# Optimization experiments

Hardware: AMD Instinct MI355X
Metric: run time of the kernel (lower is better)

Reference implementation:

```python
import jax, jax.numpy as jnp
import numpy as np

N = 50000
E = 625000
D_IN = 128
D_OUT = 128


def setup_inputs() -> dict:
    key = jax.random.key(0)
    k1, k2, k3, k4 = jax.random.split(key, 4)
    x = jax.random.normal(k1, (N, D_IN), dtype=jnp.float32)
    edge_index = jax.random.randint(k2, (2, E), 0, N, dtype=jnp.int64)
    edge_weight = jax.random.uniform(k3, (E,), dtype=jnp.float32)
    # xavier_uniform with gain=0.05: limit = gain * sqrt(6/(fan_in+fan_out))
    limit = 0.05 * np.sqrt(6.0 / (D_IN + D_OUT))
    weight = jax.random.uniform(k4, (D_OUT, D_IN), dtype=jnp.float32,
                                minval=-limit, maxval=limit)
    bias = jnp.zeros((D_OUT,), dtype=jnp.float32)
    return {"x": x, "edge_index": edge_index, "edge_weight": edge_weight,
            "weight": weight, "bias": bias}


def reference(x, edge_index, edge_weight, weight, bias):
    src = edge_index[0]
    dst = edge_index[1]
    # gather source features and weight per edge: [E, D_IN]
    msg = x[src] * edge_weight[:, None]
    # scatter-add into destination nodes: [N, D_IN]
    agg = jax.ops.segment_sum(msg, dst, num_segments=x.shape[0])
    # linear + bias + relu
    h = agg @ weight.T + bias
    return jax.nn.relu(h)
```

## Files before the change

### kernel.cpp

```cpp
#include <hip/hip_runtime.h>
#include <hip/hip_fp16.h>

#define NN 50000
#define NE 625000
#define D  128
#define CAP 64
#define NBIN 196
#define BCAP 4096
#define BIN_BLOCKS 200
#define BIN_CHUNK 3125
#define GBM 128
#define XC_BLKS 3125
#define K2_X  NBIN
#define K2_W  (NBIN + XC_BLKS)
#define K2_GRID (K2_W + 8)

typedef __attribute__((ext_vector_type(8))) short bf16x8;
typedef __attribute__((ext_vector_type(4))) float f32x4;

__device__ inline unsigned f2bf_rne(float f) {
    unsigned u = __float_as_uint(f);
    u += 0x7FFFu + ((u >> 16) & 1u);
    return u >> 16;
}

__device__ inline unsigned pack_hi(float a, float b, float& ra, float& rb) {
    unsigned ba = __float_as_uint(a) & 0xffff0000u;
    unsigned bb = __float_as_uint(b) & 0xffff0000u;
    ra = a - __uint_as_float(ba);
    rb = b - __uint_as_float(bb);
    return (ba >> 16) | bb;
}
__device__ inline unsigned pack_lo(float ra, float rb) {
    return (__float_as_uint(ra) >> 16) | (__float_as_uint(rb) & 0xffff0000u);
}

__global__ __launch_bounds__(256) void bin_coarse(const int* __restrict__ src,
                                                  const int* __restrict__ dst,
                                                  const float* __restrict__ ew,
                                                  int* __restrict__ binc,
                                                  uint2* __restrict__ binbuf,
                                                  int* __restrict__ ovf_cnt,
                                                  uint2* __restrict__ ovf) {
    __shared__ int hcnt[4][NBIN];
    __shared__ int hbase4[4][NBIN];
    __shared__ int hcur4[4][NBIN];
    const int tid = threadIdx.x;
    const int wv = tid >> 6;
    const int e0 = blockIdx.x * BIN_CHUNK;
    const int e1 = min(e0 + BIN_CHUNK, NE);

    for (int i = tid; i < NBIN; i += 256) {
        hcnt[0][i] = 0; hcnt[1][i] = 0; hcnt[2][i] = 0; hcnt[3][i] = 0;
    }
    __syncthreads();
    for (int e = e0 + tid; e < e1; e += 256)
        atomicAdd(&hcnt[wv][dst[e] >> 8], 1);
    __syncthreads();
    for (int i = tid; i < NBIN; i += 256) {
        int c0 = hcnt[0][i], c1 = hcnt[1][i], c2 = hcnt[2][i], c3 = hcnt[3][i];
        int tot = c0 + c1 + c2 + c3;
        int base = tot ? atomicAdd(&binc[i], tot) : 0;
        hbase4[0][i] = base;
        hbase4[1][i] = base + c0;
        hbase4[2][i] = base + c0 + c1;
        hbase4[3][i] = base + c0 + c1 + c2;
        hcur4[0][i] = 0; hcur4[1][i] = 0; hcur4[2][i] = 0; hcur4[3][i] = 0;
    }
    __syncthreads();
    for (int e = e0 + tid; e < e1; e += 256) {
        int d = dst[e];
        int bin = d >> 8;
        unsigned entry = ((unsigned)src[e] << 16) |
                         (unsigned)__half_as_ushort(__float2half(ew[e]));
        int slot = hbase4[wv][bin] + atomicAdd(&hcur4[wv][bin], 1);
        if (slot < BCAP) {
            binbuf[(size_t)bin * BCAP + slot] = make_uint2((unsigned)d, entry);
        } else {
            int o = atomicAdd(ovf_cnt, 1);
            ovf[o] = make_uint2((unsigned)d, entry);
        }
    }
}

__global__ __launch_bounds__(256) void k2(const float* __restrict__ x,
                                          const float* __restrict__ W,
                                          const int* __restrict__ binc,
                                          const uint2* __restrict__ binbuf,
                                          int* __restrict__ fillc,
                                          unsigned* __restrict__ buck,
                                          unsigned* __restrict__ xb,
                                          ushort* __restrict__ wsp,
                                          int* __restrict__ ovf_cnt,
                                          uint2* __restrict__ ovf) {
    const int tid = threadIdx.x;
    if (blockIdx.x < K2_X) {
        __shared__ int lcnt[256];
        const int bin = blockIdx.x;
        lcnt[tid] = 0;
        __syncthreads();
        int n = binc[bin];
        if (n > BCAP) n = BCAP;
        const uint2* bp = binbuf + (size_t)bin * BCAP;
        for (int i = tid; i < n; i += 256) {
            uint2 q = bp[i];
            int d = (int)q.x;
            int p = atomicAdd(&lcnt[d & 255], 1);
            if (p < CAP) {
                buck[(size_t)d * CAP + p] = q.y;
            } else {
                int o = atomicAdd(ovf_cnt, 1);
                ovf[o] = q;
            }
        }
        __syncthreads();
        int node = bin * 256 + tid;
        if (node < NN) {
            int c = lcnt[tid];
            if (c > CAP) c = CAP;
            int pc = (c <= 16) ? 16 : ((c + 3) & ~3);
            for (int p = c; p < pc; ++p)
                buck[(size_t)node * CAP + p] = 0;
            fillc[node] = pc;
        }
        return;
    }
    if (blockIdx.x < K2_W) {
        int g = (blockIdx.x - K2_X) * 256 + tid;
        const float4* xp = (const float4*)(x + (size_t)g * 8);
        float4 a = xp[0], b = xp[1];
        uint4 o;
        o.x = f2bf_rne(a.x) | (f2bf_rne(a.y) << 16);
        o.y = f2bf_rne(a.z) | (f2bf_rne(a.w) << 16);
        o.z = f2bf_rne(b.x) | (f2bf_rne(b.y) << 16);
        o.w = f2bf_rne(b.z) | (f2bf_rne(b.w) << 16);
        ((uint4*)xb)[g] = o;
        return;
    }
    int g = (blockIdx.x - K2_W) * 256 + tid;
    if (g >= 128 * 16) return;
    int col = g >> 4;
    int c16 = g & 15;
    const float4* wp = (const float4*)(W + (size_t)col * D + c16 * 8);
    float4 v0 = wp[0], v1 = wp[1];
    float r0, r1, r2, r3, r4, r5, r6, r7;
    uint4 hi, lo;
    hi.x = pack_hi(v0.x, v0.y, r0, r1);
    hi.y = pack_hi(v0.z, v0.w, r2, r3);
    hi.z = pack_hi(v1.x, v1.y, r4, r5);
    hi.w = pack_hi(v1.z, v1.w, r6, r7);
    lo.x = pack_lo(r0, r1); lo.y = pack_lo(r2, r3);
    lo.z = pack_lo(r4, r5); lo.w = pack_lo(r6, r7);
    int sidx = col * 16 + (c16 ^ (col & 15));
    ((uint4*)wsp)[sidx] = hi;
    ((uint4*)(wsp + 16384))[sidx] = lo;
}

__device__ inline float hw(unsigned q) {
    return __half2float(__ushort_as_half((ushort)(q & 0xffffu)));
}

__device__ inline void edge_fma(float4& acc, uint2 u, float wt) {
    acc.x += __uint_as_float(u.x << 16) * wt;
    acc.y += __uint_as_float(u.x & 0xffff0000u) * wt;
    acc.z += __uint_as_float(u.y << 16) * wt;
    acc.w += __uint_as_float(u.y & 0xffff0000u) * wt;
}

__global__ __launch_bounds__(256) void aggregate(const unsigned* __restrict__ xb,
                                                 const int* __restrict__ fillc,
                                                 const unsigned* __restrict__ buck,
                                                 const int* __restrict__ ovf_cnt,
                                                 const uint2* __restrict__ ovf,
                                                 unsigned* __restrict__ aggb) {
    const int node = blockIdx.x * 8 + (threadIdx.x >> 5);
    const int t = threadIdx.x & 31;
    int cnt = fillc[node];
    const uint4* bp4 = (const uint4*)(buck + (size_t)node * CAP);
    const uint2* x2 = (const uint2*)xb;
    float4 acc = {0.f, 0.f, 0.f, 0.f};
    if (cnt <= 16) {
        uint4 q0 = bp4[0], q1 = bp4[1], q2 = bp4[2], q3 = bp4[3];
        uint2 u00 = x2[(size_t)(q0.x >> 16) * 32 + t];
        uint2 u01 = x2[(size_t)(q0.y >> 16) * 32 + t];
        uint2 u02 = x2[(size_t)(q0.z >> 16) * 32 + t];
        uint2 u03 = x2[(size_t)(q0.w >> 16) * 32 + t];
        uint2 u10 = x2[(size_t)(q1.x >> 16) * 32 + t];
        uint2 u11 = x2[(size_t)(q1.y >> 16) * 32 + t];
        uint2 u12 = x2[(size_t)(q1.z >> 16) * 32 + t];
        uint2 u13 = x2[(size_t)(q1.w >> 16) * 32 + t];
        uint2 u20 = x2[(size_t)(q2.x >> 16) * 32 + t];
        uint2 u21 = x2[(size_t)(q2.y >> 16) * 32 + t];
        uint2 u22 = x2[(size_t)(q2.z >> 16) * 32 + t];
        uint2 u23 = x2[(size_t)(q2.w >> 16) * 32 + t];
        uint2 u30 = x2[(size_t)(q3.x >> 16) * 32 + t];
        uint2 u31 = x2[(size_t)(q3.y >> 16) * 32 + t];
        uint2 u32 = x2[(size_t)(q3.z >> 16) * 32 + t];
        uint2 u33 = x2[(size_t)(q3.w >> 16) * 32 + t];
        edge_fma(acc, u00, hw(q0.x)); edge_fma(acc, u01, hw(q0.y));
        edge_fma(acc, u02, hw(q0.z)); edge_fma(acc, u03, hw(q0.w));
        edge_fma(acc, u10, hw(q1.x)); edge_fma(acc, u11, hw(q1.y));
        edge_fma(acc, u12, hw(q1.z)); edge_fma(acc, u13, hw(q1.w));
        edge_fma(acc, u20, hw(q2.x)); edge_fma(acc, u21, hw(q2.y));
        edge_fma(acc, u22, hw(q2.z)); edge_fma(acc, u23, hw(q2.w));
        edge_fma(acc, u30, hw(q3.x)); edge_fma(acc, u31, hw(q3.y));
        edge_fma(acc, u32, hw(q3.z)); edge_fma(acc, u33, hw(q3.w));
    } else {
        int n4 = cnt >> 2;
        for (int i = 0; i < n4; ++i) {
            uint4 q = bp4[i];
            uint2 u0 = x2[(size_t)(q.x >> 16) * 32 + t];
            uint2 u1 = x2[(size_t)(q.y >> 16) * 32 + t];
            uint2 u2 = x2[(size_t)(q.z >> 16) * 32 + t];
            uint2 u3 = x2[(size_t)(q.w >> 16) * 32 + t];
            edge_fma(acc, u0, hw(q.x)); edge_fma(acc, u1, hw(q.y));
            edge_fma(acc, u2, hw(q.z)); edge_fma(acc, u3, hw(q.w));
        }
    }
    int n = *ovf_cnt;
    for (int o = 0; o < n; ++o) {
        uint2 q = ovf[o];
        if ((int)q.x == node) {
            uint2 u = x2[(size_t)(q.y >> 16) * 32 + t];
            edge_fma(acc, u, hw(q.y));
        }
    }
    unsigned o0 = f2bf_rne(acc.x) | (f2bf_rne(acc.y) << 16);
    unsigned o1 = f2bf_rne(acc.z) | (f2bf_rne(acc.w) << 16);
    ((uint2*)aggb)[(size_t)node * 32 + t] = make_uint2(o0, o1);
}

__global__ __launch_bounds__(256) void gemm_mfma(const unsigned* __restrict__ aggb,
                                                 const ushort* __restrict__ wsp,
                                                 const float* __restrict__ bias,
                                                 float* __restrict__ out) {
    __shared__ ushort wl[32768];
    const int tid = threadIdx.x;
    {
        const uint4* s = (const uint4*)wsp;
        uint4* d = (uint4*)wl;
#pragma unroll
        for (int i = 0; i < 16; ++i)
            d[i * 256 + tid] = s[i * 256 + tid];
    }
    __syncthreads();

    const int wid = tid >> 6, lane = tid & 63;
    const int l15 = lane & 15, kg = lane >> 4;
    const int wrbase = blockIdx.x * GBM + wid * 32;

    f32x4 acc[2][8];
    const f32x4 fz = {0.f, 0.f, 0.f, 0.f};
#pragma unroll
    for (int m = 0; m < 2; ++m)
#pragma unroll
        for (int n = 0; n < 8; ++n) acc[m][n] = fz;

    int arow0 = wrbase + l15;
    int arow1 = wrbase + 16 + l15;
    const unsigned* a0p = aggb + (size_t)(arow0 < NN ? arow0 : NN - 1) * 64 + kg * 4;
    const unsigned* a1p = aggb + (size_t)(arow1 < NN ? arow1 : NN - 1) * 64 + kg * 4;

#pragma unroll
    for (int kk = 0; kk < 4; ++kk) {
        uint4 h0 = *(const uint4*)(a0p + kk * 16);
        uint4 h1 = *(const uint4*)(a1p + kk * 16);
        bf16x8 a0 = *(bf16x8*)&h0;
        bf16x8 a1 = *(bf16x8*)&h1;

        int coff = ((kk * 4 + kg) ^ l15) * 8;
#pragma unroll
        for (int nf = 0; nf < 8; ++nf) {
            int bidx = (16 * nf + l15) * 128 + coff;
            bf16x8 bhi = *(const bf16x8*)&wl[bidx];
            bf16x8 blo = *(const bf16x8*)&wl[16384 + bidx];
            acc[0][nf] = __builtin_amdgcn_mfma_f32_16x16x32_bf16(a0, bhi, acc[0][nf], 0, 0, 0);
            acc[1][nf] = __builtin_amdgcn_mfma_f32_16x16x32_bf16(a1, bhi, acc[1][nf], 0, 0, 0);
            acc[0][nf] = __builtin_amdgcn_mfma_f32_16x16x32_bf16(a0, blo, acc[0][nf], 0, 0, 0);
            acc[1][nf] = __builtin_amdgcn_mfma_f32_16x16x32_bf16(a1, blo, acc[1][nf], 0, 0, 0);
        }
    }

    const int rofs = kg * 4;
#pragma unroll
    for (int nf = 0; nf < 8; ++nf) {
        int col = 16 * nf + l15;
        float bv = bias[col];
#pragma unroll
        for (int m = 0; m < 2; ++m) {
#pragma unroll
            for (int r = 0; r < 4; ++r) {
                int row = wrbase + 16 * m + rofs + r;
                if (row < NN) {
                    float h = acc[m][nf][r] + bv;
                    out[(size_t)row * D + col] = h > 0.f ? h : 0.f;
                }
            }
        }
    }
}

extern "C" void kernel_launch(void* const* d_in, const int* in_sizes, int n_in,
                              void* d_out, int out_size, void* d_ws, size_t ws_size,
                              hipStream_t stream) {
    const float* x    = (const float*)d_in[0];
    const int*   eidx = (const int*)d_in[1];
    const float* ew   = (const float*)d_in[2];
    const float* W    = (const float*)d_in[3];
    const float* bias = (const float*)d_in[4];
    float* out = (float*)d_out;

    const int* src = eidx;
    const int* dst = eidx + NE;

    char* base = (char*)d_ws;
    unsigned* aggb   = (unsigned*)base;
    uint2*    binbuf = (uint2*)base;
    unsigned* buck   = (unsigned*)(base + 25600000);
    unsigned* xb     = (unsigned*)(base + 25600000 + 12800000);
    ushort*   wsp    = (ushort*)(base + 51200000);
    int*      fillc   = (int*)(base + 51200000 + 65536);
    int*      binc    = (int*)(base + 51200000 + 65536 + 200000);
    int*      ovf_cnt = (int*)((char*)binc + NBIN * 4);
    uint2*    ovf     = (uint2*)(base + 51200000 + 65536 + 200000 + 1024);

    hipMemsetAsync(binc, 0, NBIN * 4 + 4, stream);
    bin_coarse<<<BIN_BLOCKS, 256, 0, stream>>>(src, dst, ew, binc, binbuf, ovf_cnt, ovf);
    k2<<<K2_GRID, 256, 0, stream>>>(x, W, binc, binbuf, fillc, buck, xb, wsp, ovf_cnt, ovf);
    aggregate<<<6250, 256, 0, stream>>>(xb, fillc, buck, ovf_cnt, ovf, aggb);
    gemm_mfma<<<(NN + GBM - 1) / GBM, 256, 0, stream>>>(aggb, wsp, bias, out);
}
```

Measured before the change: 82.33 us.

## Fuse fine binning into aggregation via LDS buckets and merge coarse binning with conversion

Coarse edge binning now runs in the same launch as the x and W bf16 conversion. The fine per-node bucketing and the gather-aggregate are fused into one kernel per 256-node bin, which keeps the buckets in 64KB of LDS instead of writing and re-reading a global bucket array and fill counts. This removes a kernel launch and the global bucket traffic. The cost is that aggregation now runs on only 196 blocks with large LDS use, which cuts parallelism and occupancy for the gather-heavy phase. Each block also pads its per-node work to rounds of 16 edges.

```diff
diff --git a/kernel.cpp b/kernel.cpp
--- a/kernel.cpp
+++ b/kernel.cpp
@@ -11,9 +11,9 @@
 #define BIN_CHUNK 3125
 #define GBM 128
 #define XC_BLKS 3125
-#define K2_X  NBIN
-#define K2_W  (NBIN + XC_BLKS)
-#define K2_GRID (K2_W + 8)
+#define K1_X  BIN_BLOCKS
+#define K1_W  (BIN_BLOCKS + XC_BLKS)
+#define K1_GRID (K1_W + 8)
 
 typedef __attribute__((ext_vector_type(8))) short bf16x8;
 typedef __attribute__((ext_vector_type(4))) float f32x4;
@@ -35,98 +35,71 @@
     return (__float_as_uint(ra) >> 16) | (__float_as_uint(rb) & 0xffff0000u);
 }
 
-__global__ __launch_bounds__(256) void bin_coarse(const int* __restrict__ src,
-                                                  const int* __restrict__ dst,
-                                                  const float* __restrict__ ew,
-                                                  int* __restrict__ binc,
-                                                  uint2* __restrict__ binbuf,
-                                                  int* __restrict__ ovf_cnt,
-                                                  uint2* __restrict__ ovf) {
-    __shared__ int hcnt[4][NBIN];
-    __shared__ int hbase4[4][NBIN];
-    __shared__ int hcur4[4][NBIN];
-    const int tid = threadIdx.x;
-    const int wv = tid >> 6;
-    const int e0 = blockIdx.x * BIN_CHUNK;
-    const int e1 = min(e0 + BIN_CHUNK, NE);
-
-    for (int i = tid; i < NBIN; i += 256) {
-        hcnt[0][i] = 0; hcnt[1][i] = 0; hcnt[2][i] = 0; hcnt[3][i] = 0;
-    }
-    __syncthreads();
-    for (int e = e0 + tid; e < e1; e += 256)
-        atomicAdd(&hcnt[wv][dst[e] >> 8], 1);
-    __syncthreads();
-    for (int i = tid; i < NBIN; i += 256) {
-        int c0 = hcnt[0][i], c1 = hcnt[1][i], c2 = hcnt[2][i], c3 = hcnt[3][i];
-        int tot = c0 + c1 + c2 + c3;
-        int base = tot ? atomicAdd(&binc[i], tot) : 0;
-        hbase4[0][i] = base;
-        hbase4[1][i] = base + c0;
-        hbase4[2][i] = base + c0 + c1;
-        hbase4[3][i] = base + c0 + c1 + c2;
-        hcur4[0][i] = 0; hcur4[1][i] = 0; hcur4[2][i] = 0; hcur4[3][i] = 0;
-    }
-    __syncthreads();
-    for (int e = e0 + tid; e < e1; e += 256) {
-        int d = dst[e];
-        int bin = d >> 8;
-        unsigned entry = ((unsigned)src[e] << 16) |
-                         (unsigned)__half_as_ushort(__float2half(ew[e]));
-        int slot = hbase4[wv][bin] + atomicAdd(&hcur4[wv][bin], 1);
-        if (slot < BCAP) {
-            binbuf[(size_t)bin * BCAP + slot] = make_uint2((unsigned)d, entry);
-        } else {
-            int o = atomicAdd(ovf_cnt, 1);
-            ovf[o] = make_uint2((unsigned)d, entry);
-        }
-    }
-}
-
-__global__ __launch_bounds__(256) void k2(const float* __restrict__ x,
+__device__ inline float hw(unsigned q) {
+    return __half2float(__ushort_as_half((ushort)(q & 0xffffu)));
+}
+
+__device__ inline void edge_fma(float4& acc, uint2 u, float wt) {
+    acc.x += __uint_as_float(u.x << 16) * wt;
+    acc.y += __uint_as_float(u.x & 0xffff0000u) * wt;
+    acc.z += __uint_as_float(u.y << 16) * wt;
+    acc.w += __uint_as_float(u.y & 0xffff0000u) * wt;
+}
+
+__global__ __launch_bounds__(256) void k1(const float* __restrict__ x,
                                           const float* __restrict__ W,
-                                          const int* __restrict__ binc,
-                                          const uint2* __restrict__ binbuf,
-                                          int* __restrict__ fillc,
-                                          unsigned* __restrict__ buck,
+                                          const int* __restrict__ src,
+                                          const int* __restrict__ dst,
+                                          const float* __restrict__ ew,
                                           unsigned* __restrict__ xb,
                                           ushort* __restrict__ wsp,
+                                          int* __restrict__ binc,
+                                          uint2* __restrict__ binbuf,
                                           int* __restrict__ ovf_cnt,
                                           uint2* __restrict__ ovf) {
     const int tid = threadIdx.x;
-    if (blockIdx.x < K2_X) {
-        __shared__ int lcnt[256];
-        const int bin = blockIdx.x;
-        lcnt[tid] = 0;
+    if (blockIdx.x < K1_X) {
+        __shared__ int hcnt[4][NBIN];
+        __shared__ int hbase4[4][NBIN];
+        __shared__ int hcur4[4][NBIN];
+        const int wv = tid >> 6;
+        const int e0 = blockIdx.x * BIN_CHUNK;
+        const int e1 = min(e0 + BIN_CHUNK, NE);
+        for (int i = tid; i < NBIN; i += 256) {
+            hcnt[0][i] = 0; hcnt[1][i] = 0; hcnt[2][i] = 0; hcnt[3][i] = 0;
+        }
         __syncthreads();
-        int n = binc[bin];
-        if (n > BCAP) n = BCAP;
-        const uint2* bp = binbuf + (size_t)bin * BCAP;
-        for (int i = tid; i < n; i += 256) {
-            uint2 q = bp[i];
-            int d = (int)q.x;
-            int p = atomicAdd(&lcnt[d & 255], 1);
-            if (p < CAP) {
-                buck[(size_t)d * CAP + p] = q.y;
+        for (int e = e0 + tid; e < e1; e += 256)
+            atomicAdd(&hcnt[wv][dst[e] >> 8], 1);
+        __syncthreads();
+        for (int i = tid; i < NBIN; i += 256) {
+            int c0 = hcnt[0][i], c1 = hcnt[1][i], c2 = hcnt[2][i], c3 = hcnt[3][i];
+            int tot = c0 + c1 + c2 + c3;
+            int base = tot ? atomicAdd(&binc[i], tot) : 0;
+            hbase4[0][i] = base;
+            hbase4[1][i] = base + c0;
+            hbase4[2][i] = base + c0 + c1;
+            hbase4[3][i] = base + c0 + c1 + c2;
+            hcur4[0][i] = 0; hcur4[1][i] = 0; hcur4[2][i] = 0; hcur4[3][i] = 0;
+        }
+        __syncthreads();
+        for (int e = e0 + tid; e < e1; e += 256) {
+            int d = dst[e];
+            int bin = d >> 8;
+            unsigned entry = ((unsigned)src[e] << 16) |
+                             (unsigned)__half_as_ushort(__float2half(ew[e]));
+            int slot = hbase4[wv][bin] + atomicAdd(&hcur4[wv][bin], 1);
+            if (slot < BCAP) {
+                binbuf[(size_t)bin * BCAP + slot] = make_uint2((unsigned)d, entry);
             } else {
                 int o = atomicAdd(ovf_cnt, 1);
-                ovf[o] = q;
+                ovf[o] = make_uint2((unsigned)d, entry);
             }
         }
-        __syncthreads();
-        int node = bin * 256 + tid;
-        if (node < NN) {
-            int c = lcnt[tid];
-            if (c > CAP) c = CAP;
-            int pc = (c <= 16) ? 16 : ((c + 3) & ~3);
-            for (int p = c; p < pc; ++p)
-                buck[(size_t)node * CAP + p] = 0;
-            fillc[node] = pc;
-        }
         return;
     }
-    if (blockIdx.x < K2_W) {
-        int g = (blockIdx.x - K2_X) * 256 + tid;
+    if (blockIdx.x < K1_W) {
+        int g = (blockIdx.x - K1_X) * 256 + tid;
         const float4* xp = (const float4*)(x + (size_t)g * 8);
         float4 a = xp[0], b = xp[1];
         uint4 o;
@@ -137,7 +110,7 @@
         ((uint4*)xb)[g] = o;
         return;
     }
-    int g = (blockIdx.x - K2_W) * 256 + tid;
+    int g = (blockIdx.x - K1_W) * 256 + tid;
     if (g >= 128 * 16) return;
     int col = g >> 4;
     int c16 = g & 15;
@@ -156,78 +129,90 @@
     ((uint4*)(wsp + 16384))[sidx] = lo;
 }
 
-__device__ inline float hw(unsigned q) {
-    return __half2float(__ushort_as_half((ushort)(q & 0xffffu)));
-}
-
-__device__ inline void edge_fma(float4& acc, uint2 u, float wt) {
-    acc.x += __uint_as_float(u.x << 16) * wt;
-    acc.y += __uint_as_float(u.x & 0xffff0000u) * wt;
-    acc.z += __uint_as_float(u.y << 16) * wt;
-    acc.w += __uint_as_float(u.y & 0xffff0000u) * wt;
-}
-
-__global__ __launch_bounds__(256) void aggregate(const unsigned* __restrict__ xb,
-                                                 const int* __restrict__ fillc,
-                                                 const unsigned* __restrict__ buck,
-                                                 const int* __restrict__ ovf_cnt,
-                                                 const uint2* __restrict__ ovf,
-                                                 unsigned* __restrict__ aggb) {
-    const int node = blockIdx.x * 8 + (threadIdx.x >> 5);
-    const int t = threadIdx.x & 31;
-    int cnt = fillc[node];
-    const uint4* bp4 = (const uint4*)(buck + (size_t)node * CAP);
+__global__ __launch_bounds__(256) void bin_agg(const int* __restrict__ binc,
+                                               const uint2* __restrict__ binbuf,
+                                               const unsigned* __restrict__ xb,
+                                               int* __restrict__ ovf_cnt,
+                                               uint2* __restrict__ ovf,
+                                               unsigned* __restrict__ aggb) {
+    __shared__ unsigned lbuck[256 * CAP];
+    __shared__ int lcnt[256];
+    const int tid = threadIdx.x;
+    const int bin = blockIdx.x;
+    {
+        uint4* lb4 = (uint4*)lbuck;
+#pragma unroll
+        for (int i = 0; i < 256 * CAP / 4 / 256; ++i)
+            lb4[i * 256 + tid] = make_uint4(0u, 0u, 0u, 0u);
+        lcnt[tid] = 0;
+    }
+    __syncthreads();
+    int n = binc[bin];
+    if (n > BCAP) n = BCAP;
+    const uint2* bp = binbuf + (size_t)bin * BCAP;
+    for (int i = tid; i < n; i += 256) {
+        uint2 q = bp[i];
+        int lidx = (int)(q.x & 255u);
+        int p = atomicAdd(&lcnt[lidx], 1);
+        if (p < CAP) {
+            lbuck[lidx * CAP + p] = q.y;
+        } else {
+            int o = atomicAdd(ovf_cnt, 1);
+            ovf[o] = q;
+        }
+    }
+    __syncthreads();
+    const int hwv = tid >> 5;
+    const int t = tid & 31;
     const uint2* x2 = (const uint2*)xb;
-    float4 acc = {0.f, 0.f, 0.f, 0.f};
-    if (cnt <= 16) {
-        uint4 q0 = bp4[0], q1 = bp4[1], q2 = bp4[2], q3 = bp4[3];
-        uint2 u00 = x2[(size_t)(q0.x >> 16) * 32 + t];
-        uint2 u01 = x2[(size_t)(q0.y >> 16) * 32 + t];
-        uint2 u02 = x2[(size_t)(q0.z >> 16) * 32 + t];
-        uint2 u03 = x2[(size_t)(q0.w >> 16) * 32 + t];
-        uint2 u10 = x2[(size_t)(q1.x >> 16) * 32 + t];
-        uint2 u11 = x2[(size_t)(q1.y >> 16) * 32 + t];
-        uint2 u12 = x2[(size_t)(q1.z >> 16) * 32 + t];
-        uint2 u13 = x2[(size_t)(q1.w >> 16) * 32 + t];
-        uint2 u20 = x2[(size_t)(q2.x >> 16) * 32 + t];
-        uint2 u21 = x2[(size_t)(q2.y >> 16) * 32 + t];
-        uint2 u22 = x2[(size_t)(q2.z >> 16) * 32 + t];
-        uint2 u23 = x2[(size_t)(q2.w >> 16) * 32 + t];
-        uint2 u30 = x2[(size_t)(q3.x >> 16) * 32 + t];
-        uint2 u31 = x2[(size_t)(q3.y >> 16) * 32 + t];
-        uint2 u32 = x2[(size_t)(q3.z >> 16) * 32 + t];
-        uint2 u33 = x2[(size_t)(q3.w >> 16) * 32 + t];
-        edge_fma(acc, u00, hw(q0.x)); edge_fma(acc, u01, hw(q0.y));
-        edge_fma(acc, u02, hw(q0.z)); edge_fma(acc, u03, hw(q0.w));
-        edge_fma(acc, u10, hw(q1.x)); edge_fma(acc, u11, hw(q1.y));
-        edge_fma(acc, u12, hw(q1.z)); edge_fma(acc, u13, hw(q1.w));
-        edge_fma(acc, u20, hw(q2.x)); edge_fma(acc, u21, hw(q2.y));
-        edge_fma(acc, u22, hw(q2.z)); edge_fma(acc, u23, hw(q2.w));
-        edge_fma(acc, u30, hw(q3.x)); edge_fma(acc, u31, hw(q3.y));
-        edge_fma(acc, u32, hw(q3.z)); edge_fma(acc, u33, hw(q3.w));
-    } else {
-        int n4 = cnt >> 2;
-        for (int i = 0; i < n4; ++i) {
-            uint4 q = bp4[i];
-            uint2 u0 = x2[(size_t)(q.x >> 16) * 32 + t];
-            uint2 u1 = x2[(size_t)(q.y >> 16) * 32 + t];
-            uint2 u2 = x2[(size_t)(q.z >> 16) * 32 + t];
-            uint2 u3 = x2[(size_t)(q.w >> 16) * 32 + t];
-            edge_fma(acc, u0, hw(q.x)); edge_fma(acc, u1, hw(q.y));
-            edge_fma(acc, u2, hw(q.z)); edge_fma(acc, u3, hw(q.w));
-        }
-    }
-    int n = *ovf_cnt;
-    for (int o = 0; o < n; ++o) {
-        uint2 q = ovf[o];
-        if ((int)q.x == node) {
-            uint2 u = x2[(size_t)(q.y >> 16) * 32 + t];
-            edge_fma(acc, u, hw(q.y));
-        }
-    }
-    unsigned o0 = f2bf_rne(acc.x) | (f2bf_rne(acc.y) << 16);
-    unsigned o1 = f2bf_rne(acc.z) | (f2bf_rne(acc.w) << 16);
-    ((uint2*)aggb)[(size_t)node * 32 + t] = make_uint2(o0, o1);
+    const int novf = *ovf_cnt;
+    for (int lidx = hwv; lidx < 256; lidx += 8) {
+        int node = bin * 256 + lidx;
+        if (node >= NN) continue;
+        int c = lcnt[lidx];
+        if (c > CAP) c = CAP;
+        float4 acc = {0.f, 0.f, 0.f, 0.f};
+        const uint4* lb4 = (const uint4*)(lbuck + lidx * CAP);
+        int rounds = (c + 15) >> 4;
+        for (int r = 0; r < rounds; ++r) {
+            uint4 q0 = lb4[r * 4 + 0], q1 = lb4[r * 4 + 1];
+            uint4 q2 = lb4[r * 4 + 2], q3 = lb4[r * 4 + 3];
+            uint2 u00 = x2[(size_t)(q0.x >> 16) * 32 + t];
+            uint2 u01 = x2[(size_t)(q0.y >> 16) * 32 + t];
+            uint2 u02 = x2[(size_t)(q0.z >> 16) * 32 + t];
+            uint2 u03 = x2[(size_t)(q0.w >> 16) * 32 + t];
+            uint2 u10 = x2[(size_t)(q1.x >> 16) * 32 + t];
+            uint2 u11 = x2[(size_t)(q1.y >> 16) * 32 + t];
+            uint2 u12 = x2[(size_t)(q1.z >> 16) * 32 + t];
+            uint2 u13 = x2[(size_t)(q1.w >> 16) * 32 + t];
+            uint2 u20 = x2[(size_t)(q2.x >> 16) * 32 + t];
+            uint2 u21 = x2[(size_t)(q2.y >> 16) * 32 + t];
+            uint2 u22 = x2[(size_t)(q2.z >> 16) * 32 + t];
+            uint2 u23 = x2[(size_t)(q2.w >> 16) * 32 + t];
+            uint2 u30 = x2[(size_t)(q3.x >> 16) * 32 + t];
+            uint2 u31 = x2[(size_t)(q3.y >> 16) * 32 + t];
+            uint2 u32 = x2[(size_t)(q3.z >> 16) * 32 + t];
+            uint2 u33 = x2[(size_t)(q3.w >> 16) * 32 + t];
+            edge_fma(acc, u00, hw(q0.x)); edge_fma(acc, u01, hw(q0.y));
+            edge_fma(acc, u02, hw(q0.z)); edge_fma(acc, u03, hw(q0.w));
+            edge_fma(acc, u10, hw(q1.x)); edge_fma(acc, u11, hw(q1.y));
+            edge_fma(acc, u12, hw(q1.z)); edge_fma(acc, u13, hw(q1.w));
+            edge_fma(acc, u20, hw(q2.x)); edge_fma(acc, u21, hw(q2.y));
+            edge_fma(acc, u22, hw(q2.z)); edge_fma(acc, u23, hw(q2.w));
+            edge_fma(acc, u30, hw(q3.x)); edge_fma(acc, u31, hw(q3.y));
+            edge_fma(acc, u32, hw(q3.z)); edge_fma(acc, u33, hw(q3.w));
+        }
+        for (int o = 0; o < novf; ++o) {
+            uint2 q = ovf[o];
+            if ((int)q.x == node) {
+                uint2 u = x2[(size_t)(q.y >> 16) * 32 + t];
+                edge_fma(acc, u, hw(q.y));
+            }
+        }
+        unsigned o0 = f2bf_rne(acc.x) | (f2bf_rne(acc.y) << 16);
+        unsigned o1 = f2bf_rne(acc.z) | (f2bf_rne(acc.w) << 16);
+        ((uint2*)aggb)[(size_t)node * 32 + t] = make_uint2(o0, o1);
+    }
 }
 
 __global__ __launch_bounds__(256) void gemm_mfma(const unsigned* __restrict__ aggb,
@@ -315,18 +300,15 @@
 
     char* base = (char*)d_ws;
     unsigned* aggb   = (unsigned*)base;
-    uint2*    binbuf = (uint2*)base;
-    unsigned* buck   = (unsigned*)(base + 25600000);
-    unsigned* xb     = (unsigned*)(base + 25600000 + 12800000);
-    ushort*   wsp    = (ushort*)(base + 51200000);
-    int*      fillc   = (int*)(base + 51200000 + 65536);
-    int*      binc    = (int*)(base + 51200000 + 65536 + 200000);
+    uint2*    binbuf = (uint2*)(base + 12800000);
+    unsigned* xb     = (unsigned*)(base + 19300000);
+    ushort*   wsp    = (ushort*)(base + 32100000);
+    int*      binc    = (int*)(base + 32200000);
     int*      ovf_cnt = (int*)((char*)binc + NBIN * 4);
-    uint2*    ovf     = (uint2*)(base + 51200000 + 65536 + 200000 + 1024);
+    uint2*    ovf     = (uint2*)(base + 32201024);
 
     hipMemsetAsync(binc, 0, NBIN * 4 + 4, stream);
-    bin_coarse<<<BIN_BLOCKS, 256, 0, stream>>>(src, dst, ew, binc, binbuf, ovf_cnt, ovf);
-    k2<<<K2_GRID, 256, 0, stream>>>(x, W, binc, binbuf, fillc, buck, xb, wsp, ovf_cnt, ovf);
-    aggregate<<<6250, 256, 0, stream>>>(xb, fillc, buck, ovf_cnt, ovf, aggb);
+    k1<<<K1_GRID, 256, 0, stream>>>(x, W, src, dst, ew, xb, wsp, binc, binbuf, ovf_cnt, ovf);
+    bin_agg<<<NBIN, 256, 0, stream>>>(binc, binbuf, xb, ovf_cnt, ovf, aggb);
     gemm_mfma<<<(NN + GBM - 1) / GBM, 256, 0, stream>>>(aggb, wsp, bias, out);
 }
```

After: 92.38 us. +12.2%, slower.
